# Optimization experiments

Measured on AMD Instinct MI355X. Metric: run time of the kernel, lower is better.

The kernel has to match this reference:

```python
import jax, jax.numpy as jnp
import numpy as np

NUM_HEADS = 32
NUM_KV_HEADS = 8
HEAD_DIM = 128
ATTN_SCALE = 0.08838834764831845  # 1/sqrt(128)
CONTEXT_LEN = 8192
BLOCK_SIZE = 16
NUM_BLOCKS = 1024  # physical blocks -> 16384 cache slots


def setup_inputs() -> dict:
    key = jax.random.key(0)
    ks = jax.random.split(key, 6)
    q = jax.random.normal(ks[0], (1, NUM_HEADS, HEAD_DIM), jnp.float32)
    k = jax.random.normal(ks[1], (1, NUM_KV_HEADS, HEAD_DIM), jnp.float32)
    v = jax.random.normal(ks[2], (1, NUM_KV_HEADS, HEAD_DIM), jnp.float32)
    num_slots = NUM_BLOCKS * BLOCK_SIZE
    k_cache = jax.random.normal(ks[3], (num_slots, NUM_KV_HEADS, HEAD_DIM), jnp.float32)
    v_cache = jax.random.normal(ks[4], (num_slots, NUM_KV_HEADS, HEAD_DIM), jnp.float32)
    num_logical = CONTEXT_LEN // BLOCK_SIZE
    block_table = jax.random.permutation(ks[5], NUM_BLOCKS)[:num_logical].astype(jnp.int32)
    # new token is written at logical position context_len - 1
    last = CONTEXT_LEN - 1
    slot_mapping = (block_table[last // BLOCK_SIZE] * BLOCK_SIZE + last % BLOCK_SIZE)[None].astype(jnp.int32)
    return {"q": q, "k": k, "v": v, "k_cache": k_cache, "v_cache": v_cache,
            "block_table": block_table, "slot_mapping": slot_mapping,
            "context_len": CONTEXT_LEN, "block_size": BLOCK_SIZE}


def reference(q, k, v, k_cache, v_cache, block_table, slot_mapping, context_len, block_size):
    # _write_to_cache: scatter the new token's K/V into the paged cache
    k_cache = k_cache.at[slot_mapping].set(k)
    v_cache = v_cache.at[slot_mapping].set(v)
    # _build_full_slot_mapping + _read_from_cache: gather full context K/V
    pos = jnp.arange(context_len)
    slots = block_table[pos // block_size] * block_size + pos % block_size  # (S,)
    k_all = k_cache[slots]  # (S, Hkv, D)
    v_all = v_cache[slots]
    # GQA: repeat_interleave KV heads to match query heads
    g = NUM_HEADS // NUM_KV_HEADS
    k_all = jnp.repeat(k_all, g, axis=1)  # (S, H, D)
    v_all = jnp.repeat(v_all, g, axis=1)
    # manual masked SDPA; num_query_tokens == 1 -> mask is all-ones (no tril)
    scores = jnp.einsum('qhd,khd->hqk', q, k_all) * ATTN_SCALE  # (H, 1, S)
    weights = jax.nn.softmax(scores, axis=-1)
    out = jnp.einsum('hqk,khd->qhd', weights, v_all)  # (1, H, D)
    return out
```

## Files before the change

### kernel.cpp

```cpp
#include <hip/hip_runtime.h>
#include <math.h>


#define NUM_HEADS    32
#define NUM_KV_HEADS 8
#define GQA          4
#define HEAD_DIM     128
#define ATTN_SCALE   0.08838834764831845f
#define CTX          8192
#define BLK          16
#define SPLITS       256
#define CHUNK        (CTX / SPLITS)
#define PPH          4

__global__ __launch_bounds__(256, 4) void attn_partial(
    const float* __restrict__ q,
    const float* __restrict__ knew,
    const float* __restrict__ vnew,
    const float* __restrict__ kc,
    const float* __restrict__ vc,
    const int*   __restrict__ bt,
    float*       __restrict__ o_part,
    float2*      __restrict__ ml_part)
{
    const int split = blockIdx.x;
    const int kvh   = blockIdx.y;
    const int tid   = threadIdx.x;
    const int wave  = tid >> 6;
    const int lane  = tid & 63;
    const int half  = lane >> 5;
    const int l     = lane & 31;

    const int bt0 = bt[split * 2];
    const int bt1 = bt[split * 2 + 1];

    float4 qf[GQA];
#pragma unroll
    for (int h = 0; h < GQA; ++h)
        qf[h] = *(const float4*)(q + (kvh * GQA + h) * HEAD_DIM + l * 4);

    const int pbase = wave * (2 * PPH) + half;
    float4 kf[PPH], vf[PPH];
#pragma unroll
    for (int it = 0; it < PPH; ++it) {
        const int off = pbase + it * 2;
        const int pos = split * CHUNK + off;
        const int blk = (off >> 4) ? bt1 : bt0;
        const int slot = blk * BLK + (pos & 15);
        const float* kptr;
        const float* vptr;
        if (pos == CTX - 1) {
            kptr = knew + kvh * HEAD_DIM;
            vptr = vnew + kvh * HEAD_DIM;
        } else {
            const size_t row = ((size_t)slot * NUM_KV_HEADS + kvh) * HEAD_DIM;
            kptr = kc + row;
            vptr = vc + row;
        }
        kf[it] = *(const float4*)(kptr + l * 4);
        vf[it] = *(const float4*)(vptr + l * 4);
    }

    float s[PPH][GQA];
#pragma unroll
    for (int it = 0; it < PPH; ++it)
#pragma unroll
        for (int h = 0; h < GQA; ++h)
            s[it][h] = qf[h].x * kf[it].x + qf[h].y * kf[it].y +
                       qf[h].z * kf[it].z + qf[h].w * kf[it].w;

#pragma unroll
    for (int off = 16; off >= 1; off >>= 1)
#pragma unroll
        for (int it = 0; it < PPH; ++it)
#pragma unroll
            for (int h = 0; h < GQA; ++h)
                s[it][h] += __shfl_xor(s[it][h], off, 64);

    float  m[GQA], lsum[GQA];
    float4 o[GQA];
#pragma unroll
    for (int h = 0; h < GQA; ++h) {
        m[h] = -INFINITY; lsum[h] = 0.f;
        o[h] = make_float4(0.f, 0.f, 0.f, 0.f);
    }
#pragma unroll
    for (int it = 0; it < PPH; ++it) {
#pragma unroll
        for (int h = 0; h < GQA; ++h) {
            const float sc    = s[it][h] * ATTN_SCALE;
            const float mn    = fmaxf(m[h], sc);
            const float alpha = __expf(m[h] - mn);
            const float p     = __expf(sc - mn);
            m[h] = mn;
            lsum[h] = lsum[h] * alpha + p;
            o[h].x = o[h].x * alpha + p * vf[it].x;
            o[h].y = o[h].y * alpha + p * vf[it].y;
            o[h].z = o[h].z * alpha + p * vf[it].z;
            o[h].w = o[h].w * alpha + p * vf[it].w;
        }
    }

    __shared__ float lds_o[8][GQA][HEAD_DIM];
    __shared__ float lds_m[8][GQA];
    __shared__ float lds_l[8][GQA];

    const int halfid = tid >> 5;
#pragma unroll
    for (int h = 0; h < GQA; ++h) {
        *(float4*)&lds_o[halfid][h][l * 4] = o[h];
        if (l == 0) { lds_m[halfid][h] = m[h]; lds_l[halfid][h] = lsum[h]; }
    }
    __syncthreads();

    if (tid < HEAD_DIM) {
        const int d = tid;
#pragma unroll
        for (int h = 0; h < GQA; ++h) {
            float M = -INFINITY;
#pragma unroll
            for (int i = 0; i < 8; ++i) M = fmaxf(M, lds_m[i][h]);
            float acc = 0.f, L = 0.f;
#pragma unroll
            for (int i = 0; i < 8; ++i) {
                const float w = __expf(lds_m[i][h] - M);
                L   += w * lds_l[i][h];
                acc += w * lds_o[i][h][d];
            }
            const int head = kvh * GQA + h;
            o_part[((size_t)head * SPLITS + split) * HEAD_DIM + d] = acc;
            if (d == 0) ml_part[head * SPLITS + split] = make_float2(M, L);
        }
    }
}

__global__ __launch_bounds__(128) void attn_reduce(
    const float*  __restrict__ o_part,
    const float2* __restrict__ ml_part,
    float*        __restrict__ out)
{
    const int h = blockIdx.x;
    const int d = threadIdx.x;

    __shared__ float2 mls[SPLITS];
    for (int s = d; s < SPLITS; s += 128) mls[s] = ml_part[h * SPLITS + s];
    __syncthreads();

    float M = -INFINITY;
#pragma unroll 8
    for (int s = 0; s < SPLITS; ++s) M = fmaxf(M, mls[s].x);

    float acc = 0.f, L = 0.f;
#pragma unroll 8
    for (int s = 0; s < SPLITS; ++s) {
        const float w = __expf(mls[s].x - M);
        L   += w * mls[s].y;
        acc += w * o_part[((size_t)h * SPLITS + s) * HEAD_DIM + d];
    }
    out[h * HEAD_DIM + d] = acc / L;
}

extern "C" void kernel_launch(void* const* d_in, const int* in_sizes, int n_in,
                              void* d_out, int out_size, void* d_ws, size_t ws_size,
                              hipStream_t stream) {
    const float* q    = (const float*)d_in[0];
    const float* knew = (const float*)d_in[1];
    const float* vnew = (const float*)d_in[2];
    const float* kc   = (const float*)d_in[3];
    const float* vc   = (const float*)d_in[4];
    const int*   bt   = (const int*)d_in[5];

    float*  o_part  = (float*)d_ws;
    float2* ml_part = (float2*)((char*)d_ws + (size_t)NUM_HEADS * SPLITS * HEAD_DIM * sizeof(float));

    attn_partial<<<dim3(SPLITS, NUM_KV_HEADS), 256, 0, stream>>>(
        q, knew, vnew, kc, vc, bt, o_part, ml_part);
    attn_reduce<<<NUM_HEADS, HEAD_DIM, 0, stream>>>(o_part, ml_part, (float*)d_out);
}
```

Measured before the change: 174.6 us.

## Use one cache block per split and add two-stage split reduction

Doubles the number of context splits so each workgroup handles a single 16-token cache block, with each half-wave loading two positions and doing a direct two-element softmax. The single final reduction over splits is replaced by a two-level reduction: 8 split groups per head reduce partials in parallel, then a small kernel merges the 8 group results. The aim is more parallelism in the partial pass and a shorter serial loop in the reduce. In exchange it writes twice as many partial outputs and adds a third kernel launch.

```diff
diff --git a/kernel.cpp b/kernel.cpp
--- a/kernel.cpp
+++ b/kernel.cpp
@@ -9,9 +9,9 @@
 #define ATTN_SCALE   0.08838834764831845f
 #define CTX          8192
 #define BLK          16
-#define SPLITS       256
-#define CHUNK        (CTX / SPLITS)
-#define PPH          4
+#define SPLITS       512
+#define SG           8
+#define SPS          (SPLITS / SG)
 
 __global__ __launch_bounds__(256, 4) void attn_partial(
     const float* __restrict__ q,
@@ -26,86 +26,71 @@
     const int split = blockIdx.x;
     const int kvh   = blockIdx.y;
     const int tid   = threadIdx.x;
-    const int wave  = tid >> 6;
-    const int lane  = tid & 63;
-    const int half  = lane >> 5;
-    const int l     = lane & 31;
-
-    const int bt0 = bt[split * 2];
-    const int bt1 = bt[split * 2 + 1];
+    const int halfid = tid >> 5;
+    const int l      = tid & 31;
+
+    const int btE = bt[split];
 
     float4 qf[GQA];
 #pragma unroll
     for (int h = 0; h < GQA; ++h)
         qf[h] = *(const float4*)(q + (kvh * GQA + h) * HEAD_DIM + l * 4);
 
-    const int pbase = wave * (2 * PPH) + half;
-    float4 kf[PPH], vf[PPH];
-#pragma unroll
-    for (int it = 0; it < PPH; ++it) {
-        const int off = pbase + it * 2;
-        const int pos = split * CHUNK + off;
-        const int blk = (off >> 4) ? bt1 : bt0;
-        const int slot = blk * BLK + (pos & 15);
+    float4 kf[2], vf[2];
+#pragma unroll
+    for (int j = 0; j < 2; ++j) {
+        const int off = halfid * 2 + j;
         const float* kptr;
         const float* vptr;
-        if (pos == CTX - 1) {
+        if (split == SPLITS - 1 && off == 15) {
             kptr = knew + kvh * HEAD_DIM;
             vptr = vnew + kvh * HEAD_DIM;
         } else {
-            const size_t row = ((size_t)slot * NUM_KV_HEADS + kvh) * HEAD_DIM;
+            const size_t row = (((size_t)btE * BLK + off) * NUM_KV_HEADS + kvh) * HEAD_DIM;
             kptr = kc + row;
             vptr = vc + row;
         }
-        kf[it] = *(const float4*)(kptr + l * 4);
-        vf[it] = *(const float4*)(vptr + l * 4);
-    }
-
-    float s[PPH][GQA];
-#pragma unroll
-    for (int it = 0; it < PPH; ++it)
+        kf[j] = *(const float4*)(kptr + l * 4);
+        vf[j] = *(const float4*)(vptr + l * 4);
+    }
+
+    float s[2][GQA];
+#pragma unroll
+    for (int j = 0; j < 2; ++j)
 #pragma unroll
         for (int h = 0; h < GQA; ++h)
-            s[it][h] = qf[h].x * kf[it].x + qf[h].y * kf[it].y +
-                       qf[h].z * kf[it].z + qf[h].w * kf[it].w;
+            s[j][h] = qf[h].x * kf[j].x + qf[h].y * kf[j].y +
+                      qf[h].z * kf[j].z + qf[h].w * kf[j].w;
 
 #pragma unroll
     for (int off = 16; off >= 1; off >>= 1)
 #pragma unroll
-        for (int it = 0; it < PPH; ++it)
+        for (int j = 0; j < 2; ++j)
 #pragma unroll
             for (int h = 0; h < GQA; ++h)
-                s[it][h] += __shfl_xor(s[it][h], off, 64);
+                s[j][h] += __shfl_xor(s[j][h], off, 64);
 
     float  m[GQA], lsum[GQA];
     float4 o[GQA];
 #pragma unroll
     for (int h = 0; h < GQA; ++h) {
-        m[h] = -INFINITY; lsum[h] = 0.f;
-        o[h] = make_float4(0.f, 0.f, 0.f, 0.f);
-    }
-#pragma unroll
-    for (int it = 0; it < PPH; ++it) {
-#pragma unroll
-        for (int h = 0; h < GQA; ++h) {
-            const float sc    = s[it][h] * ATTN_SCALE;
-            const float mn    = fmaxf(m[h], sc);
-            const float alpha = __expf(m[h] - mn);
-            const float p     = __expf(sc - mn);
-            m[h] = mn;
-            lsum[h] = lsum[h] * alpha + p;
-            o[h].x = o[h].x * alpha + p * vf[it].x;
-            o[h].y = o[h].y * alpha + p * vf[it].y;
-            o[h].z = o[h].z * alpha + p * vf[it].z;
-            o[h].w = o[h].w * alpha + p * vf[it].w;
-        }
+        const float s0 = s[0][h] * ATTN_SCALE;
+        const float s1 = s[1][h] * ATTN_SCALE;
+        const float mn = fmaxf(s0, s1);
+        const float p0 = __expf(s0 - mn);
+        const float p1 = __expf(s1 - mn);
+        m[h]    = mn;
+        lsum[h] = p0 + p1;
+        o[h].x = p0 * vf[0].x + p1 * vf[1].x;
+        o[h].y = p0 * vf[0].y + p1 * vf[1].y;
+        o[h].z = p0 * vf[0].z + p1 * vf[1].z;
+        o[h].w = p0 * vf[0].w + p1 * vf[1].w;
     }
 
     __shared__ float lds_o[8][GQA][HEAD_DIM];
     __shared__ float lds_m[8][GQA];
     __shared__ float lds_l[8][GQA];
 
-    const int halfid = tid >> 5;
 #pragma unroll
     for (int h = 0; h < GQA; ++h) {
         *(float4*)&lds_o[halfid][h][l * 4] = o[h];
@@ -134,28 +119,58 @@
     }
 }
 
-__global__ __launch_bounds__(128) void attn_reduce(
+__global__ __launch_bounds__(128) void attn_reduce1(
     const float*  __restrict__ o_part,
     const float2* __restrict__ ml_part,
+    float*        __restrict__ o2,
+    float2*       __restrict__ ml2)
+{
+    const int h  = blockIdx.x;
+    const int sg = blockIdx.y;
+    const int d  = threadIdx.x;
+    const int s0 = sg * SPS;
+
+    __shared__ float2 mls[SPS];
+    if (d < SPS) mls[d] = ml_part[h * SPLITS + s0 + d];
+    __syncthreads();
+
+    float M = -INFINITY;
+#pragma unroll 8
+    for (int s = 0; s < SPS; ++s) M = fmaxf(M, mls[s].x);
+
+    float acc = 0.f, L = 0.f;
+#pragma unroll 8
+    for (int s = 0; s < SPS; ++s) {
+        const float w = __expf(mls[s].x - M);
+        L   += w * mls[s].y;
+        acc += w * o_part[((size_t)h * SPLITS + s0 + s) * HEAD_DIM + d];
+    }
+    o2[((size_t)h * SG + sg) * HEAD_DIM + d] = acc;
+    if (d == 0) ml2[h * SG + sg] = make_float2(M, L);
+}
+
+__global__ __launch_bounds__(128) void attn_reduce2(
+    const float*  __restrict__ o2,
+    const float2* __restrict__ ml2,
     float*        __restrict__ out)
 {
     const int h = blockIdx.x;
     const int d = threadIdx.x;
 
-    __shared__ float2 mls[SPLITS];
-    for (int s = d; s < SPLITS; s += 128) mls[s] = ml_part[h * SPLITS + s];
+    __shared__ float2 mls[SG];
+    if (d < SG) mls[d] = ml2[h * SG + d];
     __syncthreads();
 
     float M = -INFINITY;
-#pragma unroll 8
-    for (int s = 0; s < SPLITS; ++s) M = fmaxf(M, mls[s].x);
+#pragma unroll
+    for (int i = 0; i < SG; ++i) M = fmaxf(M, mls[i].x);
 
     float acc = 0.f, L = 0.f;
-#pragma unroll 8
-    for (int s = 0; s < SPLITS; ++s) {
-        const float w = __expf(mls[s].x - M);
-        L   += w * mls[s].y;
-        acc += w * o_part[((size_t)h * SPLITS + s) * HEAD_DIM + d];
+#pragma unroll
+    for (int i = 0; i < SG; ++i) {
+        const float w = __expf(mls[i].x - M);
+        L   += w * mls[i].y;
+        acc += w * o2[((size_t)h * SG + i) * HEAD_DIM + d];
     }
     out[h * HEAD_DIM + d] = acc / L;
 }
@@ -170,10 +185,17 @@
     const float* vc   = (const float*)d_in[4];
     const int*   bt   = (const int*)d_in[5];
 
-    float*  o_part  = (float*)d_ws;
-    float2* ml_part = (float2*)((char*)d_ws + (size_t)NUM_HEADS * SPLITS * HEAD_DIM * sizeof(float));
+    char* ws = (char*)d_ws;
+    float*  o_part  = (float*)ws;
+    ws += (size_t)NUM_HEADS * SPLITS * HEAD_DIM * sizeof(float);
+    float2* ml_part = (float2*)ws;
+    ws += (size_t)NUM_HEADS * SPLITS * sizeof(float2);
+    float*  o2      = (float*)ws;
+    ws += (size_t)NUM_HEADS * SG * HEAD_DIM * sizeof(float);
+    float2* ml2     = (float2*)ws;
 
     attn_partial<<<dim3(SPLITS, NUM_KV_HEADS), 256, 0, stream>>>(
         q, knew, vnew, kc, vc, bt, o_part, ml_part);
-    attn_reduce<<<NUM_HEADS, HEAD_DIM, 0, stream>>>(o_part, ml_part, (float*)d_out);
-}
+    attn_reduce1<<<dim3(NUM_HEADS, SG), 128, 0, stream>>>(o_part, ml_part, o2, ml2);
+    attn_reduce2<<<NUM_HEADS, 128, 0, stream>>>(o2, ml2, (float*)d_out);
+}
```

Result: faster. 158.0 us (-9.5%).
